# Kernel optimization log

Measured on AMD Instinct MI355X. Metric: run time of the kernel, lower is better.

Reference implementation:

```python
import jax, jax.numpy as jnp
import numpy as np

N, DEG, F, H, O, B = 100000, 16, 128, 128, 128, 8192


def setup_inputs() -> dict:
    key = jax.random.key(0)
    k1, k2, k3, k4, k5 = jax.random.split(key, 5)
    features = jax.random.normal(k1, (N, F), dtype=jnp.float32)
    w1 = jax.random.normal(k2, (2 * F, H), dtype=jnp.float32)
    w2 = jax.random.normal(k3, (2 * H, O), dtype=jnp.float32)
    neighbor_idx = jax.random.randint(k4, (N, DEG), 0, N, dtype=jnp.int32)
    nodes = jax.random.randint(k5, (B,), 0, N, dtype=jnp.int32)
    return {"features": features, "w1": w1, "w2": w2,
            "neighbor_idx": neighbor_idx, "nodes": nodes}


def reference(features, w1, w2, neighbor_idx, nodes):
    # Layer 1 (computed for all nodes, vectorized): mean-aggregate neighbor
    # raw features, concat with self features, project with w1.
    neigh_feat = features[neighbor_idx]                 # [N, DEG, F] gather
    agg1 = neigh_feat.mean(axis=1)                      # [N, F]
    h1 = jnp.concatenate([features, agg1], axis=-1) @ w1  # [N, H]

    # Layer 2 (batch nodes): mean-aggregate neighbor layer-1 embeddings,
    # concat with self layer-1 embedding, project with w2.
    h1_self = h1[nodes]                                 # [B, H]
    h1_neigh = h1[neighbor_idx[nodes]].mean(axis=1)     # [B, H]
    out = jnp.concatenate([h1_self, h1_neigh], axis=-1) @ w2  # [B, O]
    return out
```

## Files before the change

### kernel.cpp

```cpp
#include <hip/hip_runtime.h>


#define N_NODES 100000
#define DEG     16
#define FDIM    128
#define HDIM    128
#define B_NODES 8192

typedef __attribute__((ext_vector_type(8))) short bf16x8;
typedef __attribute__((ext_vector_type(8))) unsigned short u16x8;
typedef __attribute__((ext_vector_type(4))) float f32x4;

static __device__ __forceinline__ unsigned short f2bf(float f) {
    union { float f; unsigned u; } v; v.f = f;
    unsigned r = v.u + 0x7fff + ((v.u >> 16) & 1);
    return (unsigned short)(r >> 16);
}
static __device__ __forceinline__ float bf2f(unsigned short b) {
    union { unsigned u; float f; } v; v.u = ((unsigned)b) << 16;
    return v.f;
}

__global__ void prep_feat(const float* __restrict__ feat, unsigned short* __restrict__ fb) {
    long e = ((long)blockIdx.x * 256 + threadIdx.x) * 8;
    if (e >= (long)N_NODES * FDIM) return;
    float4 v0 = *(const float4*)(feat + e);
    float4 v1 = *(const float4*)(feat + e + 4);
    u16x8 o;
    o[0] = f2bf(v0.x); o[1] = f2bf(v0.y); o[2] = f2bf(v0.z); o[3] = f2bf(v0.w);
    o[4] = f2bf(v1.x); o[5] = f2bf(v1.y); o[6] = f2bf(v1.z); o[7] = f2bf(v1.w);
    *(u16x8*)(fb + e) = o;
}

__global__ void prep_w(const float* __restrict__ w1, const float* __restrict__ w2,
                       unsigned short* __restrict__ w1T, unsigned short* __restrict__ w2T) {
    const float* w = (blockIdx.x < 8) ? w1 : w2;
    unsigned short* wT = (blockIdx.x < 8) ? w1T : w2T;
    int kb = (blockIdx.x & 7) * 32;
    int n = threadIdx.x & 127, dk = threadIdx.x >> 7;
#pragma unroll
    for (int i = 0; i < 16; ++i) {
        int k = kb + dk * 16 + i;
        wT[n * 256 + k] = f2bf(w[k * 128 + n]);
    }
}

__global__ __launch_bounds__(256)
void g1_fused(const unsigned short* __restrict__ fb, const unsigned short* __restrict__ w1T,
              const int* __restrict__ nbr, unsigned short* __restrict__ h1) {
    __shared__ unsigned short Agg[128][136];
    const int t = threadIdx.x, wave = t >> 6, lane = t & 63;
    const int m16 = lane & 15, quad = lane >> 4;
    const int row0 = blockIdx.x * 128;
    const int colb = m16 * 8;

    for (int g = 0; g < 8; ++g) {
        int Lr = wave * 32 + g * 4 + quad;
        int node = row0 + Lr;
        float s[8] = {0.f, 0.f, 0.f, 0.f, 0.f, 0.f, 0.f, 0.f};
        if (node < N_NODES) {
            const int* idx = nbr + node * DEG;
#pragma unroll
            for (int d = 0; d < DEG; ++d) {
                int nb = idx[d];
                u16x8 v = *(const u16x8*)(fb + nb * FDIM + colb);
#pragma unroll
                for (int j = 0; j < 8; ++j) s[j] += bf2f(v[j]);
            }
        }
        u16x8 o;
#pragma unroll
        for (int j = 0; j < 8; ++j) o[j] = f2bf(s[j] * 0.0625f);
        *(u16x8*)(&Agg[Lr][colb]) = o;
    }
    __syncthreads();

    f32x4 acc[2][8] = {};
#pragma unroll
    for (int kc = 0; kc < 8; ++kc) {
        bf16x8 a[2], b[8];
#pragma unroll
        for (int mt = 0; mt < 2; ++mt) {
            int lr = wave * 32 + mt * 16 + m16;
            if (kc < 4) {
                int grow = row0 + lr;
                bf16x8 z = {};
                a[mt] = (grow < N_NODES) ? *(const bf16x8*)(fb + grow * FDIM + kc * 32 + quad * 8) : z;
            } else {
                a[mt] = *(const bf16x8*)(&Agg[lr][(kc - 4) * 32 + quad * 8]);
            }
        }
#pragma unroll
        for (int nt = 0; nt < 8; ++nt)
            b[nt] = *(const bf16x8*)(w1T + (nt * 16 + m16) * 256 + kc * 32 + quad * 8);
#pragma unroll
        for (int mt = 0; mt < 2; ++mt)
#pragma unroll
            for (int nt = 0; nt < 8; ++nt)
                acc[mt][nt] = __builtin_amdgcn_mfma_f32_16x16x32_bf16(a[mt], b[nt], acc[mt][nt], 0, 0, 0);
    }

#pragma unroll
    for (int mt = 0; mt < 2; ++mt) {
        int rbase = row0 + wave * 32 + mt * 16 + quad * 4;
#pragma unroll
        for (int reg = 0; reg < 4; ++reg) {
            int grow = rbase + reg;
            if (grow >= N_NODES) continue;
#pragma unroll
            for (int nt = 0; nt < 8; ++nt)
                h1[grow * HDIM + nt * 16 + m16] = f2bf(acc[mt][nt][reg]);
        }
    }
}

__global__ __launch_bounds__(256)
void g2_fused(const unsigned short* __restrict__ h1, const unsigned short* __restrict__ w2T,
              const int* __restrict__ nbr, const int* __restrict__ nodes,
              float* __restrict__ out) {
    __shared__ unsigned short X2[64][264];
    const int t = threadIdx.x, wave = t >> 6, lane = t & 63;
    const int m16 = lane & 15, quad = lane >> 4;
    const int b0 = blockIdx.x * 64;
    const int colb = m16 * 8;

    for (int g = 0; g < 4; ++g) {
        int Ln = wave * 16 + g * 4 + quad;
        int node = nodes[b0 + Ln];
        *(u16x8*)(&X2[Ln][colb]) = *(const u16x8*)(h1 + node * HDIM + colb);
        const int* idx = nbr + node * DEG;
        float s[8] = {0.f, 0.f, 0.f, 0.f, 0.f, 0.f, 0.f, 0.f};
#pragma unroll
        for (int d = 0; d < DEG; ++d) {
            int nb = idx[d];
            u16x8 v = *(const u16x8*)(h1 + nb * HDIM + colb);
#pragma unroll
            for (int j = 0; j < 8; ++j) s[j] += bf2f(v[j]);
        }
        u16x8 o;
#pragma unroll
        for (int j = 0; j < 8; ++j) o[j] = f2bf(s[j] * 0.0625f);
        *(u16x8*)(&X2[Ln][128 + colb]) = o;
    }
    __syncthreads();

    f32x4 acc[8] = {};
#pragma unroll
    for (int kc = 0; kc < 8; ++kc) {
        bf16x8 a = *(const bf16x8*)(&X2[wave * 16 + m16][kc * 32 + quad * 8]);
#pragma unroll
        for (int nt = 0; nt < 8; ++nt) {
            bf16x8 b = *(const bf16x8*)(w2T + (nt * 16 + m16) * 256 + kc * 32 + quad * 8);
            acc[nt] = __builtin_amdgcn_mfma_f32_16x16x32_bf16(a, b, acc[nt], 0, 0, 0);
        }
    }

#pragma unroll
    for (int nt = 0; nt < 8; ++nt)
#pragma unroll
        for (int reg = 0; reg < 4; ++reg) {
            int row = b0 + wave * 16 + quad * 4 + reg;
            out[row * 128 + nt * 16 + m16] = acc[nt][reg];
        }
}

extern "C" void kernel_launch(void* const* d_in, const int* in_sizes, int n_in,
                              void* d_out, int out_size, void* d_ws, size_t ws_size,
                              hipStream_t stream) {
    const float* feat  = (const float*)d_in[0];
    const float* w1    = (const float*)d_in[1];
    const float* w2    = (const float*)d_in[2];
    const int*   nbr   = (const int*)d_in[3];
    const int*   nodes = (const int*)d_in[4];
    float* out = (float*)d_out;

    char* ws = (char*)d_ws;
    unsigned short* fb  = (unsigned short*)ws;
    unsigned short* h1  = (unsigned short*)(ws + 25600000);
    unsigned short* w1T = (unsigned short*)(ws + 51200000);
    unsigned short* w2T = (unsigned short*)(ws + 51265536);

    prep_feat<<<6250, 256, 0, stream>>>(feat, fb);
    prep_w<<<16, 256, 0, stream>>>(w1, w2, w1T, w2T);
    g1_fused<<<(N_NODES + 127) / 128, 256, 0, stream>>>(fb, w1T, nbr, h1);
    g2_fused<<<B_NODES / 64, 256, 0, stream>>>(h1, w2T, nbr, nodes, out);
}
```

Before: 204.9 us.

## Gather neighbor features in fp8 and split aggregation from layer-1 GEMM

Features are converted to fp8 (e4m3) instead of bf16 for the neighbor gather, which halves the bytes read per random row. The layer-1 aggregation moves into its own kernel that writes a bf16 agg buffer. The GEMM now reads self features straight from fp32 and converts them inline, and the two prep kernels are merged into one launch. The costs are an extra round-trip of the agg buffer through global memory, one more launch, and lower accuracy from fp8 features, which may break tolerance.

New measurement: 185.6 us. 1.1x faster.

```diff
diff --git a/kernel.cpp b/kernel.cpp
--- a/kernel.cpp
+++ b/kernel.cpp
@@ -10,6 +10,7 @@
 typedef __attribute__((ext_vector_type(8))) short bf16x8;
 typedef __attribute__((ext_vector_type(8))) unsigned short u16x8;
 typedef __attribute__((ext_vector_type(4))) float f32x4;
+typedef __attribute__((ext_vector_type(2))) float f32x2;
 
 static __device__ __forceinline__ unsigned short f2bf(float f) {
     union { float f; unsigned u; } v; v.f = f;
@@ -21,59 +22,66 @@
     return v.f;
 }
 
-__global__ void prep_feat(const float* __restrict__ feat, unsigned short* __restrict__ fb) {
-    long e = ((long)blockIdx.x * 256 + threadIdx.x) * 8;
-    if (e >= (long)N_NODES * FDIM) return;
-    float4 v0 = *(const float4*)(feat + e);
-    float4 v1 = *(const float4*)(feat + e + 4);
+__global__ __launch_bounds__(256)
+void prep(const float* __restrict__ feat, const float* __restrict__ w1,
+          const float* __restrict__ w2, unsigned char* __restrict__ f8,
+          unsigned short* __restrict__ w1T, unsigned short* __restrict__ w2T) {
+    if (blockIdx.x < 6250) {
+        long e = ((long)blockIdx.x * 256 + threadIdx.x) * 8;
+        float4 v0 = *(const float4*)(feat + e);
+        float4 v1 = *(const float4*)(feat + e + 4);
+        int p0 = 0, p1 = 0;
+        p0 = __builtin_amdgcn_cvt_pk_fp8_f32(v0.x, v0.y, p0, false);
+        p0 = __builtin_amdgcn_cvt_pk_fp8_f32(v0.z, v0.w, p0, true);
+        p1 = __builtin_amdgcn_cvt_pk_fp8_f32(v1.x, v1.y, p1, false);
+        p1 = __builtin_amdgcn_cvt_pk_fp8_f32(v1.z, v1.w, p1, true);
+        uint2 o; o.x = (unsigned)p0; o.y = (unsigned)p1;
+        *(uint2*)(f8 + e) = o;
+    } else {
+        int bid = blockIdx.x - 6250;
+        const float* w = (bid < 8) ? w1 : w2;
+        unsigned short* wT = (bid < 8) ? w1T : w2T;
+        int kb = (bid & 7) * 32;
+        int n = threadIdx.x & 127, dk = threadIdx.x >> 7;
+#pragma unroll
+        for (int i = 0; i < 16; ++i) {
+            int k = kb + dk * 16 + i;
+            wT[n * 256 + k] = f2bf(w[k * 128 + n]);
+        }
+    }
+}
+
+__global__ __launch_bounds__(256)
+void k1_agg(const unsigned char* __restrict__ f8, const int* __restrict__ nbr,
+            unsigned short* __restrict__ agg) {
+    const int t = threadIdx.x;
+    const int node = blockIdx.x * 16 + (t >> 4);
+    const int cg = (t & 15) * 8;
+    const int* idx = nbr + node * DEG;
+    float s[8] = {0.f, 0.f, 0.f, 0.f, 0.f, 0.f, 0.f, 0.f};
+#pragma unroll
+    for (int d = 0; d < DEG; ++d) {
+        int nb = idx[d];
+        uint2 v = *(const uint2*)(f8 + (long)nb * FDIM + cg);
+        f32x2 a0 = __builtin_amdgcn_cvt_pk_f32_fp8((int)v.x, false);
+        f32x2 a1 = __builtin_amdgcn_cvt_pk_f32_fp8((int)v.x, true);
+        f32x2 a2 = __builtin_amdgcn_cvt_pk_f32_fp8((int)v.y, false);
+        f32x2 a3 = __builtin_amdgcn_cvt_pk_f32_fp8((int)v.y, true);
+        s[0] += a0[0]; s[1] += a0[1]; s[2] += a1[0]; s[3] += a1[1];
+        s[4] += a2[0]; s[5] += a2[1]; s[6] += a3[0]; s[7] += a3[1];
+    }
     u16x8 o;
-    o[0] = f2bf(v0.x); o[1] = f2bf(v0.y); o[2] = f2bf(v0.z); o[3] = f2bf(v0.w);
-    o[4] = f2bf(v1.x); o[5] = f2bf(v1.y); o[6] = f2bf(v1.z); o[7] = f2bf(v1.w);
-    *(u16x8*)(fb + e) = o;
-}
-
-__global__ void prep_w(const float* __restrict__ w1, const float* __restrict__ w2,
-                       unsigned short* __restrict__ w1T, unsigned short* __restrict__ w2T) {
-    const float* w = (blockIdx.x < 8) ? w1 : w2;
-    unsigned short* wT = (blockIdx.x < 8) ? w1T : w2T;
-    int kb = (blockIdx.x & 7) * 32;
-    int n = threadIdx.x & 127, dk = threadIdx.x >> 7;
-#pragma unroll
-    for (int i = 0; i < 16; ++i) {
-        int k = kb + dk * 16 + i;
-        wT[n * 256 + k] = f2bf(w[k * 128 + n]);
-    }
-}
-
-__global__ __launch_bounds__(256)
-void g1_fused(const unsigned short* __restrict__ fb, const unsigned short* __restrict__ w1T,
-              const int* __restrict__ nbr, unsigned short* __restrict__ h1) {
-    __shared__ unsigned short Agg[128][136];
+#pragma unroll
+    for (int j = 0; j < 8; ++j) o[j] = f2bf(s[j] * 0.0625f);
+    *(u16x8*)(agg + node * 128 + cg) = o;
+}
+
+__global__ __launch_bounds__(256)
+void g1(const float* __restrict__ feat, const unsigned short* __restrict__ agg,
+        const unsigned short* __restrict__ w1T, unsigned short* __restrict__ h1) {
     const int t = threadIdx.x, wave = t >> 6, lane = t & 63;
     const int m16 = lane & 15, quad = lane >> 4;
     const int row0 = blockIdx.x * 128;
-    const int colb = m16 * 8;
-
-    for (int g = 0; g < 8; ++g) {
-        int Lr = wave * 32 + g * 4 + quad;
-        int node = row0 + Lr;
-        float s[8] = {0.f, 0.f, 0.f, 0.f, 0.f, 0.f, 0.f, 0.f};
-        if (node < N_NODES) {
-            const int* idx = nbr + node * DEG;
-#pragma unroll
-            for (int d = 0; d < DEG; ++d) {
-                int nb = idx[d];
-                u16x8 v = *(const u16x8*)(fb + nb * FDIM + colb);
-#pragma unroll
-                for (int j = 0; j < 8; ++j) s[j] += bf2f(v[j]);
-            }
-        }
-        u16x8 o;
-#pragma unroll
-        for (int j = 0; j < 8; ++j) o[j] = f2bf(s[j] * 0.0625f);
-        *(u16x8*)(&Agg[Lr][colb]) = o;
-    }
-    __syncthreads();
 
     f32x4 acc[2][8] = {};
 #pragma unroll
@@ -81,13 +89,22 @@
         bf16x8 a[2], b[8];
 #pragma unroll
         for (int mt = 0; mt < 2; ++mt) {
-            int lr = wave * 32 + mt * 16 + m16;
-            if (kc < 4) {
-                int grow = row0 + lr;
-                bf16x8 z = {};
-                a[mt] = (grow < N_NODES) ? *(const bf16x8*)(fb + grow * FDIM + kc * 32 + quad * 8) : z;
+            int grow = row0 + wave * 32 + mt * 16 + m16;
+            bf16x8 z = {};
+            if (grow >= N_NODES) {
+                a[mt] = z;
+            } else if (kc < 4) {
+                const float* p = feat + (long)grow * 128 + kc * 32 + quad * 8;
+                float4 u0 = *(const float4*)p;
+                float4 u1 = *(const float4*)(p + 4);
+                bf16x8 c;
+                c[0] = (short)f2bf(u0.x); c[1] = (short)f2bf(u0.y);
+                c[2] = (short)f2bf(u0.z); c[3] = (short)f2bf(u0.w);
+                c[4] = (short)f2bf(u1.x); c[5] = (short)f2bf(u1.y);
+                c[6] = (short)f2bf(u1.z); c[7] = (short)f2bf(u1.w);
+                a[mt] = c;
             } else {
-                a[mt] = *(const bf16x8*)(&Agg[lr][(kc - 4) * 32 + quad * 8]);
+                a[mt] = *(const bf16x8*)(agg + (long)grow * 128 + (kc - 4) * 32 + quad * 8);
             }
         }
 #pragma unroll
@@ -175,13 +192,14 @@
     float* out = (float*)d_out;
 
     char* ws = (char*)d_ws;
-    unsigned short* fb  = (unsigned short*)ws;
-    unsigned short* h1  = (unsigned short*)(ws + 25600000);
-    unsigned short* w1T = (unsigned short*)(ws + 51200000);
-    unsigned short* w2T = (unsigned short*)(ws + 51265536);
-
-    prep_feat<<<6250, 256, 0, stream>>>(feat, fb);
-    prep_w<<<16, 256, 0, stream>>>(w1, w2, w1T, w2T);
-    g1_fused<<<(N_NODES + 127) / 128, 256, 0, stream>>>(fb, w1T, nbr, h1);
+    unsigned char*  f8  = (unsigned char*)ws;
+    unsigned short* agg = (unsigned short*)(ws + 12800000);
+    unsigned short* h1  = (unsigned short*)(ws + 38400000);
+    unsigned short* w1T = (unsigned short*)(ws + 64000000);
+    unsigned short* w2T = (unsigned short*)(ws + 64065536);
+
+    prep<<<6266, 256, 0, stream>>>(feat, w1, w2, f8, w1T, w2T);
+    k1_agg<<<6250, 256, 0, stream>>>(f8, nbr, agg);
+    g1<<<(N_NODES + 127) / 128, 256, 0, stream>>>(feat, agg, w1T, h1);
     g2_fused<<<B_NODES / 64, 256, 0, stream>>>(h1, w2T, nbr, nodes, out);
 }
```
